# Kernel optimization log

Measured on AMD Instinct MI355X. Metric: run time of the kernel, lower is better.

Reference implementation:

```python
import jax, jax.numpy as jnp
import numpy as np

N_NODES = 100000
NEG_SLOPE = 0.01  # torch F.leaky_relu default

def _degrees(edge_src, edge_dst, n):
    ones = jnp.ones(edge_src.shape[0], dtype=jnp.float32)
    dout = jax.ops.segment_sum(ones, edge_src, num_segments=n)
    din = jax.ops.segment_sum(ones, edge_dst, num_segments=n)
    # DGL clamps zero degrees to 1 (norm='both')
    dout_inv_sqrt = jax.lax.rsqrt(jnp.maximum(dout, 1.0))
    din_inv_sqrt = jax.lax.rsqrt(jnp.maximum(din, 1.0))
    return dout_inv_sqrt, din_inv_sqrt

def _graph_conv(x, W, b, edge_src, edge_dst, dout_is, din_is, n):
    # DGL GraphConv, norm='both': h_i = b + sum_{j->i} (x_j W) / sqrt(d_out(j) d_in(i))
    h = (x * dout_is[:, None]) @ W            # [N, out]
    agg = jax.ops.segment_sum(h[edge_src], edge_dst, num_segments=n)
    return agg * din_is[:, None] + b

def setup_inputs() -> dict:
    key = jax.random.key(0)
    ks = jax.random.split(key, 16)
    n, e = N_NODES, 1600000
    features = jax.random.normal(ks[0], (n, 4), dtype=jnp.float32)
    edge_src = jax.random.randint(ks[1], (e,), 0, n, dtype=jnp.int32)
    edge_dst = jax.random.randint(ks[2], (e,), 0, n, dtype=jnp.int32)
    dims = [(4, 128), (128, 128), (128, 128), (128, 128), (128, 3)]
    inp = {"features": features, "edge_src": edge_src, "edge_dst": edge_dst}
    for i, (fi, fo) in enumerate(dims):
        s = (2.0 / (fi + fo)) ** 0.5  # glorot
        inp[f"W{i+1}"] = jax.random.normal(ks[3 + i], (fi, fo), dtype=jnp.float32) * s
        inp[f"b{i+1}"] = jnp.zeros((fo,), dtype=jnp.float32)
    return inp

def reference(features, edge_src, edge_dst, W1, b1, W2, b2, W3, b3, W4, b4, W5, b5):
    n = features.shape[0]
    dout_is, din_is = _degrees(edge_src, edge_dst, n)
    lrelu = lambda x: jnp.where(x >= 0, x, NEG_SLOPE * x)
    x = lrelu(_graph_conv(features, W1, b1, edge_src, edge_dst, dout_is, din_is, n))
    x = lrelu(_graph_conv(x, W2, b2, edge_src, edge_dst, dout_is, din_is, n))
    x = lrelu(_graph_conv(x, W3, b3, edge_src, edge_dst, dout_is, din_is, n))
    x = lrelu(_graph_conv(x, W4, b4, edge_src, edge_dst, dout_is, din_is, n))
    x = _graph_conv(x, W5, b5, edge_src, edge_dst, dout_is, din_is, n)
    return x
```

## Files before the change

### kernel.cpp

```cpp
#include <hip/hip_runtime.h>
#include <hip/hip_fp16.h>
#include <math.h>


#define LRELU_SLOPE 0.01f
#define XPAD 129
#define MAXBUCK 512


__device__ inline void chunk_range(int E, int nchunks, int cid, int& lo, int& hi) {
    int chunk = (E + nchunks - 1) / nchunks;
    lo = cid * chunk;
    hi = min(E, lo + chunk);
}

__global__ __launch_bounds__(256) void k_part_hist2(const int* __restrict__ src, const int* __restrict__ dst,
                                                    int E, int nbuck,
                                                    unsigned* __restrict__ gHistS, unsigned* __restrict__ gHistD,
                                                    unsigned* __restrict__ blockBaseS, unsigned* __restrict__ blockBaseD) {
    __shared__ unsigned hs[MAXBUCK];
    __shared__ unsigned hd[MAXBUCK];
    for (int i = threadIdx.x; i < nbuck; i += 256) { hs[i] = 0u; hd[i] = 0u; }
    __syncthreads();
    int lo, hi;
    chunk_range(E, gridDim.x, blockIdx.x, lo, hi);
    for (int e = lo + threadIdx.x; e < hi; e += 256) {
        atomicAdd(&hs[src[e] >> 8], 1u);
        atomicAdd(&hd[dst[e] >> 8], 1u);
    }
    __syncthreads();
    for (int i = threadIdx.x; i < nbuck; i += 256) {
        blockBaseS[(size_t)blockIdx.x * nbuck + i] = atomicAdd(&gHistS[i], hs[i]);
        blockBaseD[(size_t)blockIdx.x * nbuck + i] = atomicAdd(&gHistD[i], hd[i]);
    }
}

__global__ __launch_bounds__(512) void k_part_scan(const unsigned* __restrict__ gHist, int nbuck,
                                                   unsigned* __restrict__ bucketStart,
                                                   unsigned* __restrict__ row_ptr_last, unsigned Eval) {
    __shared__ unsigned s[MAXBUCK];
    int t = threadIdx.x;
    s[t] = (t < nbuck) ? gHist[t] : 0u;
    __syncthreads();
    for (int off = 1; off < MAXBUCK; off <<= 1) {
        unsigned v = (t >= off) ? s[t - off] : 0u;
        __syncthreads();
        s[t] += v;
        __syncthreads();
    }
    if (t <= nbuck) bucketStart[t] = (t == 0) ? 0u : s[t - 1];
    if (t == 0 && row_ptr_last) *row_ptr_last = Eval;
}

__global__ __launch_bounds__(256) void k_part_scatter_both(const int* __restrict__ src, const int* __restrict__ dst,
                                                           int E, int nbuck,
                                                           const unsigned* __restrict__ bstartS,
                                                           const unsigned* __restrict__ bstartD,
                                                           const unsigned* __restrict__ blockBaseS,
                                                           const unsigned* __restrict__ blockBaseD,
                                                           int2* __restrict__ pairs, int* __restrict__ srcbuf) {
    __shared__ unsigned curS[MAXBUCK];
    __shared__ unsigned curD[MAXBUCK];
    for (int i = threadIdx.x; i < nbuck; i += 256) {
        curS[i] = bstartS[i] + blockBaseS[(size_t)blockIdx.x * nbuck + i];
        curD[i] = bstartD[i] + blockBaseD[(size_t)blockIdx.x * nbuck + i];
    }
    __syncthreads();
    int lo, hi;
    chunk_range(E, gridDim.x, blockIdx.x, lo, hi);
    for (int e = lo + threadIdx.x; e < hi; e += 256) {
        int s = src[e], d = dst[e];
        unsigned posD = atomicAdd(&curD[d >> 8], 1u);
        pairs[posD] = make_int2(s, d);
        unsigned posS = atomicAdd(&curS[s >> 8], 1u);
        srcbuf[posS] = s;
    }
}

__global__ __launch_bounds__(256) void k_bucket_csr(const int2* __restrict__ pairs,
                                                    const unsigned* __restrict__ bucketStart,
                                                    unsigned* __restrict__ row_ptr,
                                                    unsigned* __restrict__ din_cnt,
                                                    int* __restrict__ csr, int n) {
    __shared__ unsigned hist[256];
    __shared__ unsigned scanw[256];
    __shared__ unsigned cur[256];
    int b = blockIdx.x, t = threadIdx.x;
    unsigned beg = bucketStart[b], end = bucketStart[b + 1];
    hist[t] = 0u;
    __syncthreads();
    for (unsigned e = beg + t; e < end; e += 256)
        atomicAdd(&hist[pairs[e].y & 255], 1u);
    __syncthreads();
    scanw[t] = hist[t];
    __syncthreads();
    for (int off = 1; off < 256; off <<= 1) {
        unsigned u = (t >= off) ? scanw[t - off] : 0u;
        __syncthreads();
        scanw[t] += u;
        __syncthreads();
    }
    unsigned excl = scanw[t] - hist[t];
    int node = (b << 8) + t;
    if (node < n) {
        row_ptr[node] = beg + excl;
        din_cnt[node] = hist[t];
    }
    cur[t] = excl;
    __syncthreads();
    for (unsigned e = beg + t; e < end; e += 256) {
        int2 p = pairs[e];
        unsigned pos = beg + atomicAdd(&cur[p.y & 255], 1u);
        csr[pos] = p.x;
    }
}

__global__ __launch_bounds__(256) void k_bucket_cnt(const int* __restrict__ vals,
                                                    const unsigned* __restrict__ bucketStart,
                                                    unsigned* __restrict__ dout_cnt, int n) {
    __shared__ unsigned hist[256];
    int b = blockIdx.x, t = threadIdx.x;
    unsigned beg = bucketStart[b], end = bucketStart[b + 1];
    hist[t] = 0u;
    __syncthreads();
    for (unsigned e = beg + t; e < end; e += 256)
        atomicAdd(&hist[vals[e] & 255], 1u);
    __syncthreads();
    int node = (b << 8) + t;
    if (node < n) dout_cnt[node] = hist[t];
}

__global__ void k_invsqrt2(const unsigned* __restrict__ c0, float* __restrict__ i0,
                           const unsigned* __restrict__ c1, float* __restrict__ i1, int n) {
    int i = blockIdx.x * blockDim.x + threadIdx.x;
    if (i < n) {
        i0[i] = 1.0f / sqrtf(fmaxf((float)c0[i], 1.0f));
        i1[i] = 1.0f / sqrtf(fmaxf((float)c1[i], 1.0f));
    }
}


__global__ void k_prescale4(const float* __restrict__ x, const float* __restrict__ dout_is,
                            float* __restrict__ pf4, int n) {
    int i = blockIdx.x * blockDim.x + threadIdx.x;
    if (i >= n) return;
    float s = dout_is[i];
    float4 v = *reinterpret_cast<const float4*>(x + (size_t)i * 4);
    float4 o = {v.x * s, v.y * s, v.z * s, v.w * s};
    *reinterpret_cast<float4*>(pf4 + (size_t)i * 4) = o;
}

__global__ void k_gather4(const float* __restrict__ pf4, const int* __restrict__ csr,
                          const unsigned* __restrict__ row_ptr, const float* __restrict__ din_is,
                          const float* __restrict__ dout_is, float* __restrict__ a4, int n) {
    int i = blockIdx.x * blockDim.x + threadIdx.x;
    if (i >= n) return;
    unsigned beg = row_ptr[i], end = row_ptr[i + 1];
    float4 acc = {0.f, 0.f, 0.f, 0.f};
    unsigned e = beg;
    for (; e + 4 <= end; e += 4) {
        int s0 = csr[e], s1 = csr[e + 1], s2 = csr[e + 2], s3 = csr[e + 3];
        float4 v0 = *reinterpret_cast<const float4*>(pf4 + (size_t)s0 * 4);
        float4 v1 = *reinterpret_cast<const float4*>(pf4 + (size_t)s1 * 4);
        float4 v2 = *reinterpret_cast<const float4*>(pf4 + (size_t)s2 * 4);
        float4 v3 = *reinterpret_cast<const float4*>(pf4 + (size_t)s3 * 4);
        acc.x += (v0.x + v1.x) + (v2.x + v3.x);
        acc.y += (v0.y + v1.y) + (v2.y + v3.y);
        acc.z += (v0.z + v1.z) + (v2.z + v3.z);
        acc.w += (v0.w + v1.w) + (v2.w + v3.w);
    }
    for (; e < end; ++e) {
        int s = csr[e];
        float4 v = *reinterpret_cast<const float4*>(pf4 + (size_t)s * 4);
        acc.x += v.x; acc.y += v.y; acc.z += v.z; acc.w += v.w;
    }
    float sc = din_is[i] * dout_is[i];
    float4 o = {acc.x * sc, acc.y * sc, acc.z * sc, acc.w * sc};
    *reinterpret_cast<float4*>(a4 + (size_t)i * 4) = o;
}


__device__ inline float4 ldh4(const __half* p) {
    uint2 u = *reinterpret_cast<const uint2*>(p);
    __half2 h0 = *reinterpret_cast<const __half2*>(&u.x);
    __half2 h1 = *reinterpret_cast<const __half2*>(&u.y);
    float2 a = __half22float2(h0);
    float2 b = __half22float2(h1);
    return make_float4(a.x, a.y, b.x, b.y);
}

__device__ inline void sth16(__half* p, const float* v) {
    __half2 hh[8];
#pragma unroll
    for (int q = 0; q < 8; ++q) hh[q] = __floats2half2_rn(v[2 * q], v[2 * q + 1]);
    const float4* f = reinterpret_cast<const float4*>(&hh[0]);
    *reinterpret_cast<float4*>(p) = f[0];
    *reinterpret_cast<float4*>(p + 8) = f[1];
}


__device__ inline float4 xp1_cols(float4 av, float ds, float4 wa, float4 wb, float4 wc, float4 wd, float4 bc) {
    float4 r;
    r.x = fmaf(av.x, wa.x, fmaf(av.y, wb.x, fmaf(av.z, wc.x, fmaf(av.w, wd.x, ds * bc.x))));
    r.y = fmaf(av.x, wa.y, fmaf(av.y, wb.y, fmaf(av.z, wc.y, fmaf(av.w, wd.y, ds * bc.y))));
    r.z = fmaf(av.x, wa.z, fmaf(av.y, wb.z, fmaf(av.z, wc.z, fmaf(av.w, wd.z, ds * bc.z))));
    r.w = fmaf(av.x, wa.w, fmaf(av.y, wb.w, fmaf(av.z, wc.w, fmaf(av.w, wd.w, ds * bc.w))));
    r.x = (r.x >= 0.f) ? r.x : LRELU_SLOPE * r.x;
    r.y = (r.y >= 0.f) ? r.y : LRELU_SLOPE * r.y;
    r.z = (r.z >= 0.f) ? r.z : LRELU_SLOPE * r.z;
    r.w = (r.w >= 0.f) ? r.w : LRELU_SLOPE * r.w;
    return r;
}

__global__ __launch_bounds__(512) void k_gl12(const float* __restrict__ a4,
                                              const float* __restrict__ dout_v,
                                              const int* __restrict__ csr,
                                              const unsigned* __restrict__ row_ptr,
                                              const float* __restrict__ din_is, const float* __restrict__ dout_is,
                                              const float* __restrict__ W1, const float* __restrict__ b1,
                                              const float* __restrict__ W2, const float* __restrict__ b2,
                                              __half* __restrict__ xh_out, int n) {
    __shared__ float xs[64 * XPAD];
    const int t = threadIdx.x;
    const int bbase = blockIdx.x * 64;
    const int wave = t >> 6;
    const int lane = t & 63;
    const int half = lane >> 5;
    const int j4 = (lane & 31) * 4;

    float4 wa = *reinterpret_cast<const float4*>(W1 + 0 * 128 + j4);
    float4 wb = *reinterpret_cast<const float4*>(W1 + 1 * 128 + j4);
    float4 wc = *reinterpret_cast<const float4*>(W1 + 2 * 128 + j4);
    float4 wd = *reinterpret_cast<const float4*>(W1 + 3 * 128 + j4);
    float4 bc = *reinterpret_cast<const float4*>(b1 + j4);

#pragma unroll
    for (int sweep = 0; sweep < 4; ++sweep) {
        int r = wave * 2 + half + sweep * 16;
        int node = bbase + r;
        float4 acc = {0.f, 0.f, 0.f, 0.f};
        if (node < n) {
            unsigned beg = row_ptr[node], end = row_ptr[node + 1];
            unsigned e = beg;
            for (; e + 4 <= end; e += 4) {
                int s0 = csr[e + 0], s1 = csr[e + 1], s2 = csr[e + 2], s3 = csr[e + 3];
                float4 a0 = *reinterpret_cast<const float4*>(a4 + (size_t)s0 * 4);
                float4 a1 = *reinterpret_cast<const float4*>(a4 + (size_t)s1 * 4);
                float4 a2 = *reinterpret_cast<const float4*>(a4 + (size_t)s2 * 4);
                float4 a3 = *reinterpret_cast<const float4*>(a4 + (size_t)s3 * 4);
                float d0 = dout_v[s0], d1 = dout_v[s1], d2 = dout_v[s2], d3 = dout_v[s3];
                float4 x0 = xp1_cols(a0, d0, wa, wb, wc, wd, bc);
                float4 x1 = xp1_cols(a1, d1, wa, wb, wc, wd, bc);
                float4 x2 = xp1_cols(a2, d2, wa, wb, wc, wd, bc);
                float4 x3 = xp1_cols(a3, d3, wa, wb, wc, wd, bc);
                acc.x += (x0.x + x1.x) + (x2.x + x3.x);
                acc.y += (x0.y + x1.y) + (x2.y + x3.y);
                acc.z += (x0.z + x1.z) + (x2.z + x3.z);
                acc.w += (x0.w + x1.w) + (x2.w + x3.w);
            }
            for (; e < end; ++e) {
                int s = csr[e];
                float4 av = *reinterpret_cast<const float4*>(a4 + (size_t)s * 4);
                float4 xv = xp1_cols(av, dout_v[s], wa, wb, wc, wd, bc);
                acc.x += xv.x; acc.y += xv.y; acc.z += xv.z; acc.w += xv.w;
            }
            float di = din_is[node];
            acc.x *= di; acc.y *= di; acc.z *= di; acc.w *= di;
        }
        float* d = xs + r * XPAD + j4;
        d[0] = acc.x; d[1] = acc.y; d[2] = acc.z; d[3] = acc.w;
    }
    __syncthreads();

    const int jg = __builtin_amdgcn_readfirstlane(wave) & 7;
    const int j0 = jg * 16;
    const float* Wj = W2 + j0;
    const float* xrow = xs + lane * XPAD;

    float acc[16];
#pragma unroll
    for (int q = 0; q < 16; ++q) acc[q] = 0.f;

#pragma unroll 2
    for (int k = 0; k < 128; k += 4) {
        float x0 = xrow[k + 0];
        float x1 = xrow[k + 1];
        float x2 = xrow[k + 2];
        float x3 = xrow[k + 3];
        const float* w0 = Wj + (size_t)k * 128;
#pragma unroll
        for (int q = 0; q < 16; ++q) {
            acc[q] += x0 * w0[q] + x1 * w0[128 + q] + x2 * w0[256 + q] + x3 * w0[384 + q];
        }
    }

    int node = bbase + lane;
    if (node < n) {
        float s = dout_is[node];
        float v[16];
#pragma unroll
        for (int q = 0; q < 16; ++q) {
            float u = acc[q] + b2[j0 + q];
            u = (u >= 0.f) ? u : LRELU_SLOPE * u;
            v[q] = u * s;
        }
        sth16(xh_out + (size_t)node * 128 + j0, v);
    }
}


__global__ __launch_bounds__(512) void k_gl128h(const __half* __restrict__ xh, const int* __restrict__ csr,
                                                const unsigned* __restrict__ row_ptr,
                                                const float* __restrict__ din_is, const float* __restrict__ dout_is,
                                                const float* __restrict__ W, const float* __restrict__ b,
                                                __half* __restrict__ xh_out, float* __restrict__ xo32, int n) {
    __shared__ float xs[64 * XPAD];
    const int t = threadIdx.x;
    const int bbase = blockIdx.x * 64;
    const int wave = t >> 6;
    const int lane = t & 63;
    const int half = lane >> 5;
    const int j4 = (lane & 31) * 4;

#pragma unroll
    for (int sweep = 0; sweep < 4; ++sweep) {
        int r = wave * 2 + half + sweep * 16;
        int node = bbase + r;
        float4 accA = {0.f, 0.f, 0.f, 0.f};
        float4 accB = {0.f, 0.f, 0.f, 0.f};
        if (node < n) {
            unsigned beg = row_ptr[node], end = row_ptr[node + 1];
            unsigned e = beg;
            for (; e + 8 <= end; e += 8) {
                int s0 = csr[e + 0], s1 = csr[e + 1], s2 = csr[e + 2], s3 = csr[e + 3];
                int s4 = csr[e + 4], s5 = csr[e + 5], s6 = csr[e + 6], s7 = csr[e + 7];
                float4 v0 = ldh4(xh + (size_t)s0 * 128 + j4);
                float4 v1 = ldh4(xh + (size_t)s1 * 128 + j4);
                float4 v2 = ldh4(xh + (size_t)s2 * 128 + j4);
                float4 v3 = ldh4(xh + (size_t)s3 * 128 + j4);
                float4 v4 = ldh4(xh + (size_t)s4 * 128 + j4);
                float4 v5 = ldh4(xh + (size_t)s5 * 128 + j4);
                float4 v6 = ldh4(xh + (size_t)s6 * 128 + j4);
                float4 v7 = ldh4(xh + (size_t)s7 * 128 + j4);
                accA.x += (v0.x + v1.x) + (v2.x + v3.x);
                accA.y += (v0.y + v1.y) + (v2.y + v3.y);
                accA.z += (v0.z + v1.z) + (v2.z + v3.z);
                accA.w += (v0.w + v1.w) + (v2.w + v3.w);
                accB.x += (v4.x + v5.x) + (v6.x + v7.x);
                accB.y += (v4.y + v5.y) + (v6.y + v7.y);
                accB.z += (v4.z + v5.z) + (v6.z + v7.z);
                accB.w += (v4.w + v5.w) + (v6.w + v7.w);
            }
            if (e + 4 <= end) {
                int s0 = csr[e + 0], s1 = csr[e + 1], s2 = csr[e + 2], s3 = csr[e + 3];
                float4 v0 = ldh4(xh + (size_t)s0 * 128 + j4);
                float4 v1 = ldh4(xh + (size_t)s1 * 128 + j4);
                float4 v2 = ldh4(xh + (size_t)s2 * 128 + j4);
                float4 v3 = ldh4(xh + (size_t)s3 * 128 + j4);
                accA.x += (v0.x + v1.x) + (v2.x + v3.x);
                accA.y += (v0.y + v1.y) + (v2.y + v3.y);
                accA.z += (v0.z + v1.z) + (v2.z + v3.z);
                accA.w += (v0.w + v1.w) + (v2.w + v3.w);
                e += 4;
            }
            for (; e < end; ++e) {
                int s = csr[e];
                float4 v = ldh4(xh + (size_t)s * 128 + j4);
                accB.x += v.x; accB.y += v.y; accB.z += v.z; accB.w += v.w;
            }
            float di = din_is[node];
            accA.x = (accA.x + accB.x) * di;
            accA.y = (accA.y + accB.y) * di;
            accA.z = (accA.z + accB.z) * di;
            accA.w = (accA.w + accB.w) * di;
        }
        float* d = xs + r * XPAD + j4;
        d[0] = accA.x; d[1] = accA.y; d[2] = accA.z; d[3] = accA.w;
    }
    __syncthreads();

    const int jg = __builtin_amdgcn_readfirstlane(wave) & 7;
    const int j0 = jg * 16;
    const float* Wj = W + j0;
    const float* xrow = xs + lane * XPAD;

    float acc[16];
#pragma unroll
    for (int q = 0; q < 16; ++q) acc[q] = 0.f;

#pragma unroll 2
    for (int k = 0; k < 128; k += 4) {
        float x0 = xrow[k + 0];
        float x1 = xrow[k + 1];
        float x2 = xrow[k + 2];
        float x3 = xrow[k + 3];
        const float* w0 = Wj + (size_t)k * 128;
#pragma unroll
        for (int q = 0; q < 16; ++q) {
            acc[q] += x0 * w0[q] + x1 * w0[128 + q] + x2 * w0[256 + q] + x3 * w0[384 + q];
        }
    }

    int node = bbase + lane;
    if (node < n) {
        float s = dout_is[node];
        float v[16];
#pragma unroll
        for (int q = 0; q < 16; ++q) {
            float u = acc[q] + b[j0 + q];
            u = (u >= 0.f) ? u : LRELU_SLOPE * u;
            v[q] = u * s;
        }
        if (xh_out) sth16(xh_out + (size_t)node * 128 + j0, v);
        if (xo32) {
            float* out = xo32 + (size_t)node * 128 + j0;
#pragma unroll
            for (int q = 0; q < 16; q += 4) {
                float4 o = {v[q], v[q + 1], v[q + 2], v[q + 3]};
                *reinterpret_cast<float4*>(out + q) = o;
            }
        }
    }
}


__global__ __launch_bounds__(256) void k_lin5v(const float* __restrict__ xp, const float* __restrict__ W,
                                               float* __restrict__ h, int n) {
    int node = blockIdx.x * 8 + (threadIdx.x >> 5);
    if (node >= n) return;
    int l = threadIdx.x & 31;
    int k4 = l * 4;
    float4 xv = *reinterpret_cast<const float4*>(xp + (size_t)node * 128 + k4);
    float4 wA = *reinterpret_cast<const float4*>(W + (size_t)k4 * 3);
    float4 wB = *reinterpret_cast<const float4*>(W + (size_t)k4 * 3 + 4);
    float4 wC = *reinterpret_cast<const float4*>(W + (size_t)k4 * 3 + 8);
    float p0 = xv.x * wA.x + xv.y * wA.w + xv.z * wB.z + xv.w * wC.y;
    float p1 = xv.x * wA.y + xv.y * wB.x + xv.z * wB.w + xv.w * wC.z;
    float p2 = xv.x * wA.z + xv.y * wB.y + xv.z * wC.x + xv.w * wC.w;
    for (int off = 16; off; off >>= 1) {
        p0 += __shfl_xor(p0, off, 32);
        p1 += __shfl_xor(p1, off, 32);
        p2 += __shfl_xor(p2, off, 32);
    }
    if (l == 0) {
        h[(size_t)node * 3 + 0] = p0;
        h[(size_t)node * 3 + 1] = p1;
        h[(size_t)node * 3 + 2] = p2;
    }
}

__global__ void k_gather3(const float* __restrict__ h, const int* __restrict__ csr,
                          const unsigned* __restrict__ row_ptr, const float* __restrict__ din_is,
                          const float* __restrict__ b, float* __restrict__ out, int n) {
    int i = blockIdx.x * blockDim.x + threadIdx.x;
    if (i >= n) return;
    unsigned beg = row_ptr[i], end = row_ptr[i + 1];
    float a0 = 0.f, a1 = 0.f, a2 = 0.f;
    for (unsigned e = beg; e < end; ++e) {
        int s = csr[e];
        a0 += h[(size_t)s * 3 + 0];
        a1 += h[(size_t)s * 3 + 1];
        a2 += h[(size_t)s * 3 + 2];
    }
    float di = din_is[i];
    out[(size_t)i * 3 + 0] = a0 * di + b[0];
    out[(size_t)i * 3 + 1] = a1 * di + b[1];
    out[(size_t)i * 3 + 2] = a2 * di + b[2];
}


extern "C" void kernel_launch(void* const* d_in, const int* in_sizes, int n_in,
                              void* d_out, int out_size, void* d_ws, size_t ws_size,
                              hipStream_t stream) {
    const float* features = (const float*)d_in[0];
    const int* esrc = (const int*)d_in[1];
    const int* edst = (const int*)d_in[2];
    const float* W1 = (const float*)d_in[3];  const float* b1 = (const float*)d_in[4];
    const float* W2 = (const float*)d_in[5];  const float* b2 = (const float*)d_in[6];
    const float* W3 = (const float*)d_in[7];  const float* b3 = (const float*)d_in[8];
    const float* W4 = (const float*)d_in[9];  const float* b4 = (const float*)d_in[10];
    const float* W5 = (const float*)d_in[11]; const float* b5 = (const float*)d_in[12];

    const int N = in_sizes[0] / 4;
    const int E = in_sizes[1];
    const int nbuck = (N + 255) / 256;
    const int NPB = 256;

    size_t off = 0;
    auto carve = [&](size_t bytes) -> void* {
        void* p = (char*)d_ws + off;
        off = (off + bytes + 255) & ~(size_t)255;
        return p;
    };
    float*    A         = (float*)carve((size_t)N * 128 * 4);
    float*    Bp        = (float*)carve((size_t)N * 8 * 4);
    __half*   xh2       = (__half*)carve((size_t)N * 128 * 2);
    __half*   xh3       = (__half*)carve((size_t)N * 128 * 2);
    int*      csr       = (int*)carve((size_t)E * 4);
    unsigned* row_ptr   = (unsigned*)carve((size_t)(N + 1) * 4);
    unsigned* dout_cnt  = (unsigned*)carve((size_t)N * 4);
    unsigned* din_cnt   = (unsigned*)carve((size_t)N * 4);
    float*    dout_is   = (float*)carve((size_t)N * 4);
    float*    din_is    = (float*)carve((size_t)N * 4);
    unsigned* gHistD    = (unsigned*)carve((size_t)MAXBUCK * 4);
    unsigned* gHistS    = (unsigned*)carve((size_t)MAXBUCK * 4);
    unsigned* bstartD   = (unsigned*)carve((size_t)(MAXBUCK + 1) * 4);
    unsigned* bstartS   = (unsigned*)carve((size_t)(MAXBUCK + 1) * 4);
    unsigned* blockBaseD = (unsigned*)carve((size_t)NPB * nbuck * 4);
    unsigned* blockBaseS = (unsigned*)carve((size_t)NPB * nbuck * 4);
    float*    h5        = (float*)carve((size_t)N * 3 * 4);
    (void)ws_size;
    int2* pairs  = (int2*)A;
    int*  srcbuf = (int*)((char*)A + (size_t)E * 8);
    float* pf4 = Bp;
    float* a4  = Bp + (size_t)N * 4;

    hipMemsetAsync(gHistD, 0, (size_t)MAXBUCK * 4, stream);
    hipMemsetAsync(gHistS, 0, (size_t)MAXBUCK * 4, stream);

    k_part_hist2<<<NPB, 256, 0, stream>>>(esrc, edst, E, nbuck, gHistS, gHistD, blockBaseS, blockBaseD);
    k_part_scan<<<1, 512, 0, stream>>>(gHistD, nbuck, bstartD, row_ptr + N, (unsigned)E);
    k_part_scan<<<1, 512, 0, stream>>>(gHistS, nbuck, bstartS, (unsigned*)nullptr, 0u);
    k_part_scatter_both<<<NPB, 256, 0, stream>>>(esrc, edst, E, nbuck, bstartS, bstartD,
                                                 blockBaseS, blockBaseD, pairs, srcbuf);
    k_bucket_csr<<<nbuck, 256, 0, stream>>>(pairs, bstartD, row_ptr, din_cnt, csr, N);
    k_bucket_cnt<<<nbuck, 256, 0, stream>>>(srcbuf, bstartS, dout_cnt, N);
    k_invsqrt2<<<(N + 255) / 256, 256, 0, stream>>>(dout_cnt, dout_is, din_cnt, din_is, N);

    k_prescale4<<<(N + 255) / 256, 256, 0, stream>>>(features, dout_is, pf4, N);
    k_gather4<<<(N + 255) / 256, 256, 0, stream>>>(pf4, csr, row_ptr, din_is, dout_is, a4, N);

    int glGrid = (N + 63) / 64;
    k_gl12<<<glGrid, 512, 0, stream>>>(a4, dout_is, csr, row_ptr, din_is, dout_is, W1, b1, W2, b2, xh2, N);
    k_gl128h<<<glGrid, 512, 0, stream>>>(xh2, csr, row_ptr, din_is, dout_is, W3, b3, xh3, (float*)nullptr, N);
    k_gl128h<<<glGrid, 512, 0, stream>>>(xh3, csr, row_ptr, din_is, dout_is, W4, b4, (__half*)nullptr, A, N);

    k_lin5v<<<(N + 7) / 8, 256, 0, stream>>>(A, W5, h5, N);
    k_gather3<<<(N + 255) / 256, 256, 0, stream>>>(h5, csr, row_ptr, din_is, b5, (float*)d_out, N);
}
```

Baseline: 467.2 us.

## Widen fp16 gather loads and fuse final linear into layer-4 kernel

The 128-wide fp16 gather now has each lane load 16 bytes (8 halves), with two half-wave groups taking alternate edges and combining their partial sums through a cross-lane shuffle. The layer-4 kernel also applies the W5 projection in-kernel and reduces the three outputs across waves in shared memory. This removes the fp32 N×128 intermediate write and the separate k_lin5v pass. In exchange it adds a shared-memory reduction with extra barriers, and the summation order changes.

```diff
diff --git a/kernel.cpp b/kernel.cpp
--- a/kernel.cpp
+++ b/kernel.cpp
@@ -180,15 +180,6 @@
 }
 
 
-__device__ inline float4 ldh4(const __half* p) {
-    uint2 u = *reinterpret_cast<const uint2*>(p);
-    __half2 h0 = *reinterpret_cast<const __half2*>(&u.x);
-    __half2 h1 = *reinterpret_cast<const __half2*>(&u.y);
-    float2 a = __half22float2(h0);
-    float2 b = __half22float2(h1);
-    return make_float4(a.x, a.y, b.x, b.y);
-}
-
 __device__ inline void sth16(__half* p, const float* v) {
     __half2 hh[8];
 #pragma unroll
@@ -196,6 +187,16 @@
     const float4* f = reinterpret_cast<const float4*>(&hh[0]);
     *reinterpret_cast<float4*>(p) = f[0];
     *reinterpret_cast<float4*>(p + 8) = f[1];
+}
+
+__device__ inline void acc8(float* acc, uint4 u) {
+    const __half2* h = reinterpret_cast<const __half2*>(&u);
+#pragma unroll
+    for (int q = 0; q < 4; ++q) {
+        float2 f = __half22float2(h[q]);
+        acc[2 * q] += f.x;
+        acc[2 * q + 1] += f.y;
+    }
 }
 
 
@@ -309,74 +310,61 @@
 }
 
 
+#define GATHER_FP16_TILE(XH)                                                         \
+    for (int sweep = 0; sweep < 4; ++sweep) {                                        \
+        int r = wave * 2 + half + sweep * 16;                                        \
+        int node = bbase + r;                                                        \
+        float acc[8];                                                                \
+        _Pragma("unroll") for (int q = 0; q < 8; ++q) acc[q] = 0.f;                  \
+        float di = 0.f;                                                              \
+        if (node < n) {                                                              \
+            unsigned beg = row_ptr[node], end = row_ptr[node + 1];                   \
+            unsigned e = beg;                                                        \
+            for (; e + 8 <= end; e += 8) {                                           \
+                int s0 = csr[e + 0 + sub];                                           \
+                int s1 = csr[e + 2 + sub];                                           \
+                int s2 = csr[e + 4 + sub];                                           \
+                int s3 = csr[e + 6 + sub];                                           \
+                uint4 u0 = *reinterpret_cast<const uint4*>(XH + (size_t)s0 * 128 + c8); \
+                uint4 u1 = *reinterpret_cast<const uint4*>(XH + (size_t)s1 * 128 + c8); \
+                uint4 u2 = *reinterpret_cast<const uint4*>(XH + (size_t)s2 * 128 + c8); \
+                uint4 u3 = *reinterpret_cast<const uint4*>(XH + (size_t)s3 * 128 + c8); \
+                acc8(acc, u0); acc8(acc, u1); acc8(acc, u2); acc8(acc, u3);          \
+            }                                                                        \
+            for (; e + 2 <= end; e += 2) {                                           \
+                int s = csr[e + sub];                                                \
+                acc8(acc, *reinterpret_cast<const uint4*>(XH + (size_t)s * 128 + c8)); \
+            }                                                                        \
+            if (e < end && sub == 0) {                                               \
+                int s = csr[e];                                                      \
+                acc8(acc, *reinterpret_cast<const uint4*>(XH + (size_t)s * 128 + c8)); \
+            }                                                                        \
+            di = din_is[node];                                                       \
+        }                                                                            \
+        _Pragma("unroll") for (int q = 0; q < 8; ++q)                                \
+            acc[q] += __shfl_xor(acc[q], 16, 64);                                    \
+        if (sub == 0) {                                                              \
+            float* d = xs + r * XPAD + c8;                                           \
+            _Pragma("unroll") for (int q = 0; q < 8; ++q) d[q] = acc[q] * di;        \
+        }                                                                            \
+    }
+
+
 __global__ __launch_bounds__(512) void k_gl128h(const __half* __restrict__ xh, const int* __restrict__ csr,
                                                 const unsigned* __restrict__ row_ptr,
                                                 const float* __restrict__ din_is, const float* __restrict__ dout_is,
                                                 const float* __restrict__ W, const float* __restrict__ b,
-                                                __half* __restrict__ xh_out, float* __restrict__ xo32, int n) {
+                                                __half* __restrict__ xh_out, int n) {
     __shared__ float xs[64 * XPAD];
     const int t = threadIdx.x;
     const int bbase = blockIdx.x * 64;
     const int wave = t >> 6;
     const int lane = t & 63;
     const int half = lane >> 5;
-    const int j4 = (lane & 31) * 4;
-
-#pragma unroll
-    for (int sweep = 0; sweep < 4; ++sweep) {
-        int r = wave * 2 + half + sweep * 16;
-        int node = bbase + r;
-        float4 accA = {0.f, 0.f, 0.f, 0.f};
-        float4 accB = {0.f, 0.f, 0.f, 0.f};
-        if (node < n) {
-            unsigned beg = row_ptr[node], end = row_ptr[node + 1];
-            unsigned e = beg;
-            for (; e + 8 <= end; e += 8) {
-                int s0 = csr[e + 0], s1 = csr[e + 1], s2 = csr[e + 2], s3 = csr[e + 3];
-                int s4 = csr[e + 4], s5 = csr[e + 5], s6 = csr[e + 6], s7 = csr[e + 7];
-                float4 v0 = ldh4(xh + (size_t)s0 * 128 + j4);
-                float4 v1 = ldh4(xh + (size_t)s1 * 128 + j4);
-                float4 v2 = ldh4(xh + (size_t)s2 * 128 + j4);
-                float4 v3 = ldh4(xh + (size_t)s3 * 128 + j4);
-                float4 v4 = ldh4(xh + (size_t)s4 * 128 + j4);
-                float4 v5 = ldh4(xh + (size_t)s5 * 128 + j4);
-                float4 v6 = ldh4(xh + (size_t)s6 * 128 + j4);
-                float4 v7 = ldh4(xh + (size_t)s7 * 128 + j4);
-                accA.x += (v0.x + v1.x) + (v2.x + v3.x);
-                accA.y += (v0.y + v1.y) + (v2.y + v3.y);
-                accA.z += (v0.z + v1.z) + (v2.z + v3.z);
-                accA.w += (v0.w + v1.w) + (v2.w + v3.w);
-                accB.x += (v4.x + v5.x) + (v6.x + v7.x);
-                accB.y += (v4.y + v5.y) + (v6.y + v7.y);
-                accB.z += (v4.z + v5.z) + (v6.z + v7.z);
-                accB.w += (v4.w + v5.w) + (v6.w + v7.w);
-            }
-            if (e + 4 <= end) {
-                int s0 = csr[e + 0], s1 = csr[e + 1], s2 = csr[e + 2], s3 = csr[e + 3];
-                float4 v0 = ldh4(xh + (size_t)s0 * 128 + j4);
-                float4 v1 = ldh4(xh + (size_t)s1 * 128 + j4);
-                float4 v2 = ldh4(xh + (size_t)s2 * 128 + j4);
-                float4 v3 = ldh4(xh + (size_t)s3 * 128 + j4);
-                accA.x += (v0.x + v1.x) + (v2.x + v3.x);
-                accA.y += (v0.y + v1.y) + (v2.y + v3.y);
-                accA.z += (v0.z + v1.z) + (v2.z + v3.z);
-                accA.w += (v0.w + v1.w) + (v2.w + v3.w);
-                e += 4;
-            }
-            for (; e < end; ++e) {
-                int s = csr[e];
-                float4 v = ldh4(xh + (size_t)s * 128 + j4);
-                accB.x += v.x; accB.y += v.y; accB.z += v.z; accB.w += v.w;
-            }
-            float di = din_is[node];
-            accA.x = (accA.x + accB.x) * di;
-            accA.y = (accA.y + accB.y) * di;
-            accA.z = (accA.z + accB.z) * di;
-            accA.w = (accA.w + accB.w) * di;
-        }
-        float* d = xs + r * XPAD + j4;
-        d[0] = accA.x; d[1] = accA.y; d[2] = accA.z; d[3] = accA.w;
-    }
+    const int sub = (lane >> 4) & 1;
+    const int c8 = (lane & 15) * 8;
+
+    GATHER_FP16_TILE(xh)
     __syncthreads();
 
     const int jg = __builtin_amdgcn_readfirstlane(wave) & 7;
@@ -411,43 +399,86 @@
             u = (u >= 0.f) ? u : LRELU_SLOPE * u;
             v[q] = u * s;
         }
-        if (xh_out) sth16(xh_out + (size_t)node * 128 + j0, v);
-        if (xo32) {
-            float* out = xo32 + (size_t)node * 128 + j0;
-#pragma unroll
-            for (int q = 0; q < 16; q += 4) {
-                float4 o = {v[q], v[q + 1], v[q + 2], v[q + 3]};
-                *reinterpret_cast<float4*>(out + q) = o;
+        sth16(xh_out + (size_t)node * 128 + j0, v);
+    }
+}
+
+
+__global__ __launch_bounds__(512) void k_gl128f(const __half* __restrict__ xh, const int* __restrict__ csr,
+                                                const unsigned* __restrict__ row_ptr,
+                                                const float* __restrict__ din_is, const float* __restrict__ dout_is,
+                                                const float* __restrict__ W, const float* __restrict__ b,
+                                                const float* __restrict__ W5,
+                                                float* __restrict__ h5, int n) {
+    __shared__ float xs[64 * XPAD];
+    const int t = threadIdx.x;
+    const int bbase = blockIdx.x * 64;
+    const int wave = t >> 6;
+    const int lane = t & 63;
+    const int half = lane >> 5;
+    const int sub = (lane >> 4) & 1;
+    const int c8 = (lane & 15) * 8;
+
+    GATHER_FP16_TILE(xh)
+    __syncthreads();
+
+    const int jg = __builtin_amdgcn_readfirstlane(wave) & 7;
+    const int j0 = jg * 16;
+    const float* Wj = W + j0;
+    const float* xrow = xs + lane * XPAD;
+
+    float acc[16];
+#pragma unroll
+    for (int q = 0; q < 16; ++q) acc[q] = 0.f;
+
+#pragma unroll 2
+    for (int k = 0; k < 128; k += 4) {
+        float x0 = xrow[k + 0];
+        float x1 = xrow[k + 1];
+        float x2 = xrow[k + 2];
+        float x3 = xrow[k + 3];
+        const float* w0 = Wj + (size_t)k * 128;
+#pragma unroll
+        for (int q = 0; q < 16; ++q) {
+            acc[q] += x0 * w0[q] + x1 * w0[128 + q] + x2 * w0[256 + q] + x3 * w0[384 + q];
+        }
+    }
+
+    float s = (bbase + lane < n) ? dout_is[bbase + lane] : 0.f;
+    float p0 = 0.f, p1 = 0.f, p2 = 0.f;
+#pragma unroll
+    for (int q = 0; q < 16; ++q) {
+        float u = acc[q] + b[j0 + q];
+        u = (u >= 0.f) ? u : LRELU_SLOPE * u;
+        u *= s;
+        const float* w5r = W5 + (size_t)(j0 + q) * 3;
+        p0 = fmaf(u, w5r[0], p0);
+        p1 = fmaf(u, w5r[1], p1);
+        p2 = fmaf(u, w5r[2], p2);
+    }
+    __syncthreads();
+    float* red = xs;
+    red[lane * 24 + wave * 3 + 0] = p0;
+    red[lane * 24 + wave * 3 + 1] = p1;
+    red[lane * 24 + wave * 3 + 2] = p2;
+    __syncthreads();
+    if (t < 64) {
+        int node = bbase + t;
+        if (node < n) {
+            float a0 = 0.f, a1 = 0.f, a2 = 0.f;
+#pragma unroll
+            for (int w = 0; w < 8; ++w) {
+                a0 += red[t * 24 + w * 3 + 0];
+                a1 += red[t * 24 + w * 3 + 1];
+                a2 += red[t * 24 + w * 3 + 2];
             }
-        }
-    }
-}
-
-
-__global__ __launch_bounds__(256) void k_lin5v(const float* __restrict__ xp, const float* __restrict__ W,
-                                               float* __restrict__ h, int n) {
-    int node = blockIdx.x * 8 + (threadIdx.x >> 5);
-    if (node >= n) return;
-    int l = threadIdx.x & 31;
-    int k4 = l * 4;
-    float4 xv = *reinterpret_cast<const float4*>(xp + (size_t)node * 128 + k4);
-    float4 wA = *reinterpret_cast<const float4*>(W + (size_t)k4 * 3);
-    float4 wB = *reinterpret_cast<const float4*>(W + (size_t)k4 * 3 + 4);
-    float4 wC = *reinterpret_cast<const float4*>(W + (size_t)k4 * 3 + 8);
-    float p0 = xv.x * wA.x + xv.y * wA.w + xv.z * wB.z + xv.w * wC.y;
-    float p1 = xv.x * wA.y + xv.y * wB.x + xv.z * wB.w + xv.w * wC.z;
-    float p2 = xv.x * wA.z + xv.y * wB.y + xv.z * wC.x + xv.w * wC.w;
-    for (int off = 16; off; off >>= 1) {
-        p0 += __shfl_xor(p0, off, 32);
-        p1 += __shfl_xor(p1, off, 32);
-        p2 += __shfl_xor(p2, off, 32);
-    }
-    if (l == 0) {
-        h[(size_t)node * 3 + 0] = p0;
-        h[(size_t)node * 3 + 1] = p1;
-        h[(size_t)node * 3 + 2] = p2;
-    }
-}
+            h5[(size_t)node * 3 + 0] = a0;
+            h5[(size_t)node * 3 + 1] = a1;
+            h5[(size_t)node * 3 + 2] = a2;
+        }
+    }
+}
+
 
 __global__ void k_gather3(const float* __restrict__ h, const int* __restrict__ csr,
                           const unsigned* __restrict__ row_ptr, const float* __restrict__ din_is,
@@ -492,7 +523,7 @@
         off = (off + bytes + 255) & ~(size_t)255;
         return p;
     };
-    float*    A         = (float*)carve((size_t)N * 128 * 4);
+    char*     scratch   = (char*)carve((size_t)E * 12 + 256);
     float*    Bp        = (float*)carve((size_t)N * 8 * 4);
     __half*   xh2       = (__half*)carve((size_t)N * 128 * 2);
     __half*   xh3       = (__half*)carve((size_t)N * 128 * 2);
@@ -510,8 +541,8 @@
     unsigned* blockBaseS = (unsigned*)carve((size_t)NPB * nbuck * 4);
     float*    h5        = (float*)carve((size_t)N * 3 * 4);
     (void)ws_size;
-    int2* pairs  = (int2*)A;
-    int*  srcbuf = (int*)((char*)A + (size_t)E * 8);
+    int2* pairs  = (int2*)scratch;
+    int*  srcbuf = (int*)(scratch + (size_t)E * 8);
     float* pf4 = Bp;
     float* a4  = Bp + (size_t)N * 4;
 
@@ -532,9 +563,8 @@
 
     int glGrid = (N + 63) / 64;
     k_gl12<<<glGrid, 512, 0, stream>>>(a4, dout_is, csr, row_ptr, din_is, dout_is, W1, b1, W2, b2, xh2, N);
-    k_gl128h<<<glGrid, 512, 0, stream>>>(xh2, csr, row_ptr, din_is, dout_is, W3, b3, xh3, (float*)nullptr, N);
-    k_gl128h<<<glGrid, 512, 0, stream>>>(xh3, csr, row_ptr, din_is, dout_is, W4, b4, (__half*)nullptr, A, N);
-
-    k_lin5v<<<(N + 7) / 8, 256, 0, stream>>>(A, W5, h5, N);
+    k_gl128h<<<glGrid, 512, 0, stream>>>(xh2, csr, row_ptr, din_is, dout_is, W3, b3, xh3, N);
+    k_gl128f<<<glGrid, 512, 0, stream>>>(xh3, csr, row_ptr, din_is, dout_is, W4, b4, W5, h5, N);
+
     k_gather3<<<(N + 255) / 256, 256, 0, stream>>>(h5, csr, row_ptr, din_is, b5, (float*)d_out, N);
 }
```

Result: faster. 437.3 us (-6.4%).
